# Performance work log

Hardware: AMD Instinct MI355X
Metric: run time of the kernel (lower is better)

The kernel has to match this reference:

```python
import jax, jax.numpy as jnp
import numpy as np


def setup_inputs() -> dict:
    key = jax.random.key(0)
    ks = jax.random.split(key, 6)
    b, t, k, h = 8, 128, 128, 4
    q_x = jax.random.normal(ks[0], (b, t, k), dtype=jnp.float32)
    kv_x = jax.random.normal(ks[1], (b, t, t - 1, k), dtype=jnp.float32)
    s = 1.0 / np.sqrt(k).astype(np.float32)
    Wk = jax.random.normal(ks[2], (k, k), dtype=jnp.float32) * s  # tokeys.weight
    Wq = jax.random.normal(ks[3], (k, k), dtype=jnp.float32) * s  # toqueries.weight
    Wv = jax.random.normal(ks[4], ((1 + k) * h, 2 * k), dtype=jnp.float32) * (1.0 / np.sqrt(2 * k).astype(np.float32))  # tovalues.weight
    bv = jax.random.normal(ks[5], ((1 + k) * h,), dtype=jnp.float32) * 0.01  # tovalues.bias
    return dict(q_x=q_x, kv_x=kv_x, Wk=Wk, Wq=Wq, Wv=Wv, bv=bv)


def reference(q_x, kv_x, Wk, Wq, Wv, bv):
    # kv_x: (b, t, t-1, k); q_x: (b, t, k)
    b, t, m, k = kv_x.shape  # m == t - 1
    h = Wv.shape[0] // (k + 1)
    # torch Linear: y = x @ W.T
    keys = jnp.einsum('btmk,jk->btmj', kv_x, Wk)          # (b,t,m,k)
    queries = jnp.einsum('btk,jk->btj', q_x, Wq)          # (b,t,k)
    queries = jnp.broadcast_to(queries[:, :, None, :], (b, t, m, k))
    value_input = jnp.concatenate([keys, queries], axis=-1)  # (b,t,m,2k)
    vals = jnp.einsum('btmc,oc->btmo', value_input, Wv) + bv  # (b,t,m,(1+k)h)
    vals = vals.reshape(b, t, m, h, k + 1)
    score = vals[..., 0]        # (b,t,m,h)
    values = vals[..., 1:]      # (b,t,m,h,k)
    w = jax.nn.softmax(score, axis=2)  # softmax over the t-1 (pair) axis
    x = jnp.einsum('btmh,btmhk->bthk', w, values)  # weighted sum over pairs
    return x.reshape(b, t, h * k)
```

## Files before the change

kernel.cpp:

```cpp
#include <hip/hip_runtime.h>

#define KD 128
#define NH 4
#define MM 127
#define NO 516

#define OFF_W1S 0
#define OFF_WC  512
#define OFF_C   (512 + 131072)

__global__ void precompute_w(const float* __restrict__ Wk,
                             const float* __restrict__ Wq,
                             const float* __restrict__ Wv,
                             float* __restrict__ ws) {
    int o = blockIdx.x;
    int k = threadIdx.x;
    const float* wvrow = Wv + o * 256;
    float acc1 = 0.f, acc2 = 0.f;
    #pragma unroll 8
    for (int j = 0; j < 128; ++j) {
        acc1 += wvrow[j]       * Wk[j * 128 + k];
        acc2 += wvrow[128 + j] * Wq[j * 128 + k];
    }
    int h = o / 129;
    int r = o - h * 129;
    if (r == 0) {
        ws[OFF_W1S + h * 128 + k] = acc1;
    } else {
        int dd = r - 1;
        float* dst = ws + OFF_WC + (size_t)(h * 128 + dd) * 256;
        dst[k]       = acc1;
        dst[128 + k] = acc2;
    }
}

__global__ __launch_bounds__(256, 4)
void attn_csum(const float* __restrict__ kv_x, float* __restrict__ ws) {
    __shared__ float ssc[512];
    __shared__ float swt[512];
    __shared__ float cpart[8][512];

    const int bt  = blockIdx.x;
    const int tid = threadIdx.x;
    const int dq  = tid & 31;
    const int g   = tid >> 5;

    float4 w1s[NH];
    #pragma unroll
    for (int h = 0; h < NH; ++h)
        w1s[h] = *(const float4*)(ws + OFF_W1S + h * KD + dq * 4);

    const float4* src = (const float4*)(kv_x + (size_t)bt * MM * KD);
    float4 kvr[16];
    #pragma unroll
    for (int k = 0; k < 16; ++k) {
        int idx = tid + k * 256;
        if (idx < MM * 32) kvr[k] = src[idx];
        else               kvr[k] = make_float4(0.f, 0.f, 0.f, 0.f);
    }

    const int bit4 = (tid >> 4) & 1;
    const int bit3 = (tid >> 3) & 1;
    const int myh  = bit4 * 2 + bit3;
    #pragma unroll
    for (int k = 0; k < 16; ++k) {
        float4 kv4 = kvr[k];
        float p0 = kv4.x*w1s[0].x + kv4.y*w1s[0].y + kv4.z*w1s[0].z + kv4.w*w1s[0].w;
        float p1 = kv4.x*w1s[1].x + kv4.y*w1s[1].y + kv4.z*w1s[1].z + kv4.w*w1s[1].w;
        float p2 = kv4.x*w1s[2].x + kv4.y*w1s[2].y + kv4.z*w1s[2].z + kv4.w*w1s[2].w;
        float p3 = kv4.x*w1s[3].x + kv4.y*w1s[3].y + kv4.z*w1s[3].z + kv4.w*w1s[3].w;
        float x = bit4 ? p0 : p2;
        float y = bit4 ? p1 : p3;
        float a = (bit4 ? p2 : p0) + __shfl_xor(x, 16);
        float b = (bit4 ? p3 : p1) + __shfl_xor(y, 16);
        float z = bit3 ? a : b;
        float v = (bit3 ? b : a) + __shfl_xor(z, 8);
        v += __shfl_xor(v, 4);
        v += __shfl_xor(v, 2);
        v += __shfl_xor(v, 1);
        int m = g + 8 * k;
        if ((tid & 7) == 0 && m < MM) ssc[m * 4 + myh] = v;
    }
    __syncthreads();

    {
        int h = tid >> 6, lane = tid & 63;
        float v0 = ssc[lane * 4 + h];
        bool has1 = (lane + 64) < MM;
        float v1 = has1 ? ssc[(lane + 64) * 4 + h] : -1e30f;
        float mx = fmaxf(v0, v1);
        #pragma unroll
        for (int off = 32; off; off >>= 1) mx = fmaxf(mx, __shfl_xor(mx, off));
        float e0 = __expf(v0 - mx);
        float e1 = has1 ? __expf(v1 - mx) : 0.f;
        float s = e0 + e1;
        #pragma unroll
        for (int off = 32; off; off >>= 1) s += __shfl_xor(s, off);
        float inv = 1.f / s;
        swt[lane * 4 + h] = e0 * inv;
        swt[(lane + 64) * 4 + h] = has1 ? e1 * inv : 0.f;
    }
    __syncthreads();

    float4 cacc[NH];
    #pragma unroll
    for (int h = 0; h < NH; ++h) cacc[h] = make_float4(0.f, 0.f, 0.f, 0.f);
    #pragma unroll
    for (int k = 0; k < 16; ++k) {
        int m = g + 8 * k;
        float4 wv  = *(const float4*)&swt[m * 4];
        float4 kv4 = kvr[k];
        cacc[0].x += wv.x*kv4.x; cacc[0].y += wv.x*kv4.y; cacc[0].z += wv.x*kv4.z; cacc[0].w += wv.x*kv4.w;
        cacc[1].x += wv.y*kv4.x; cacc[1].y += wv.y*kv4.y; cacc[1].z += wv.y*kv4.z; cacc[1].w += wv.y*kv4.w;
        cacc[2].x += wv.z*kv4.x; cacc[2].y += wv.z*kv4.y; cacc[2].z += wv.z*kv4.z; cacc[2].w += wv.z*kv4.w;
        cacc[3].x += wv.w*kv4.x; cacc[3].y += wv.w*kv4.y; cacc[3].z += wv.w*kv4.z; cacc[3].w += wv.w*kv4.w;
    }
    #pragma unroll
    for (int h = 0; h < NH; ++h)
        *(float4*)&cpart[g][h * KD + dq * 4] = cacc[h];
    __syncthreads();

    float* cdst = ws + OFF_C + (size_t)bt * 512;
    #pragma unroll
    for (int rep = 0; rep < 2; ++rep) {
        int o = tid + rep * 256;
        float s = 0.f;
        #pragma unroll
        for (int gg = 0; gg < 8; ++gg) s += cpart[gg][o];
        cdst[o] = s;
    }
}

#define BM 32
#define BN 64
#define BK 64

__global__ __launch_bounds__(256, 2)
void proj_out(const float* __restrict__ q_x,
              const float* __restrict__ bv,
              const float* __restrict__ ws,
              float* __restrict__ out) {
    __shared__ float sA[BM][BK + 4];
    __shared__ float sB[BK][BN + 4];

    const int r0  = blockIdx.x * BM;
    const int dd0 = blockIdx.y * BN;
    const int h   = blockIdx.z;
    const int tid = threadIdx.x;
    const int tx  = tid & 15;
    const int ty  = tid >> 4;
    const float* cmat = ws + OFF_C;
    const float* Wc   = ws + OFF_WC;

    float acc[2][4];
    #pragma unroll
    for (int i = 0; i < 2; ++i)
        #pragma unroll
        for (int j = 0; j < 4; ++j) acc[i][j] = 0.f;

    for (int ks = 0; ks < 4; ++ks) {
        int kk0 = ks * BK;
        const float* Abase; int Astride;
        if (kk0 < 128) { Abase = cmat + h * KD + kk0; Astride = 512; }
        else           { Abase = q_x + (kk0 - 128);   Astride = KD;  }
        #pragma unroll
        for (int i = 0; i < 2; ++i) {
            int idx = tid + i * 256;
            int r = idx >> 4, c4 = idx & 15;
            float4 v = *(const float4*)(Abase + (size_t)(r0 + r) * Astride + c4 * 4);
            *(float4*)&sA[r][c4 * 4] = v;
        }
        #pragma unroll
        for (int i = 0; i < 4; ++i) {
            int idx = tid + i * 256;
            int dd = idx >> 4, c4 = idx & 15;
            float4 v = *(const float4*)(Wc + (size_t)(h * KD + dd0 + dd) * 256 + kk0 + c4 * 4);
            sB[c4 * 4 + 0][dd] = v.x;
            sB[c4 * 4 + 1][dd] = v.y;
            sB[c4 * 4 + 2][dd] = v.z;
            sB[c4 * 4 + 3][dd] = v.w;
        }
        __syncthreads();
        #pragma unroll 8
        for (int c = 0; c < BK; ++c) {
            float a0 = sA[ty * 2 + 0][c];
            float a1 = sA[ty * 2 + 1][c];
            float4 b4 = *(const float4*)&sB[c][tx * 4];
            acc[0][0] += a0 * b4.x; acc[0][1] += a0 * b4.y; acc[0][2] += a0 * b4.z; acc[0][3] += a0 * b4.w;
            acc[1][0] += a1 * b4.x; acc[1][1] += a1 * b4.y; acc[1][2] += a1 * b4.z; acc[1][3] += a1 * b4.w;
        }
        __syncthreads();
    }
    float bb[4];
    #pragma unroll
    for (int j = 0; j < 4; ++j) bb[j] = bv[h * 129 + 1 + dd0 + tx * 4 + j];
    #pragma unroll
    for (int i = 0; i < 2; ++i) {
        float4 v;
        v.x = acc[i][0] + bb[0];
        v.y = acc[i][1] + bb[1];
        v.z = acc[i][2] + bb[2];
        v.w = acc[i][3] + bb[3];
        *(float4*)(out + (size_t)(r0 + ty * 2 + i) * 512 + h * KD + dd0 + tx * 4) = v;
    }
}

extern "C" void kernel_launch(void* const* d_in, const int* in_sizes, int n_in,
                              void* d_out, int out_size, void* d_ws, size_t ws_size,
                              hipStream_t stream) {
    const float* q_x  = (const float*)d_in[0];
    const float* kv_x = (const float*)d_in[1];
    const float* Wk   = (const float*)d_in[2];
    const float* Wq   = (const float*)d_in[3];
    const float* Wv   = (const float*)d_in[4];
    const float* bv   = (const float*)d_in[5];
    float* out = (float*)d_out;
    float* ws  = (float*)d_ws;

    int bt = in_sizes[0] / KD;

    hipLaunchKernelGGL(precompute_w, dim3(NO), dim3(128), 0, stream, Wk, Wq, Wv, ws);
    hipLaunchKernelGGL(attn_csum, dim3(bt), dim3(256), 0, stream, kv_x, ws);
    hipLaunchKernelGGL(proj_out, dim3(bt / BM, KD / BN, NH), dim3(256), 0, stream,
                       q_x, bv, ws, out);
}
```

Measured before the change: 42.42 us.

## Store combined value weights transposed and halve proj_out tile width

The precomputed combined weight matrix is now written in transposed (k-major) layout, so proj_out can load B tiles with direct float4 copies into shared memory instead of four scalar transposing stores. The output tile width drops from 64 to 32 columns, with each thread computing one row by four columns. This doubles the grid and raises the occupancy hint, aiming for more parallelism on this small GEMM. The cost is less register reuse per thread and strided scalar writes in precompute_w.

```diff
diff --git a/kernel.cpp b/kernel.cpp
--- a/kernel.cpp
+++ b/kernel.cpp
@@ -28,9 +28,8 @@
         ws[OFF_W1S + h * 128 + k] = acc1;
     } else {
         int dd = r - 1;
-        float* dst = ws + OFF_WC + (size_t)(h * 128 + dd) * 256;
-        dst[k]       = acc1;
-        dst[128 + k] = acc2;
+        ws[OFF_WC + (size_t)(h * 256 + k) * 128 + dd]       = acc1;
+        ws[OFF_WC + (size_t)(h * 256 + 128 + k) * 128 + dd] = acc2;
     }
 }
 
@@ -132,10 +131,10 @@
 }
 
 #define BM 32
-#define BN 64
+#define BN 32
 #define BK 64
 
-__global__ __launch_bounds__(256, 2)
+__global__ __launch_bounds__(256, 4)
 void proj_out(const float* __restrict__ q_x,
               const float* __restrict__ bv,
               const float* __restrict__ ws,
@@ -147,16 +146,12 @@
     const int dd0 = blockIdx.y * BN;
     const int h   = blockIdx.z;
     const int tid = threadIdx.x;
-    const int tx  = tid & 15;
-    const int ty  = tid >> 4;
+    const int tx  = tid & 7;
+    const int ty  = tid >> 3;
     const float* cmat = ws + OFF_C;
-    const float* Wc   = ws + OFF_WC;
-
-    float acc[2][4];
-    #pragma unroll
-    for (int i = 0; i < 2; ++i)
-        #pragma unroll
-        for (int j = 0; j < 4; ++j) acc[i][j] = 0.f;
+    const float* Wct  = ws + OFF_WC;
+
+    float acc[4] = {0.f, 0.f, 0.f, 0.f};
 
     for (int ks = 0; ks < 4; ++ks) {
         int kk0 = ks * BK;
@@ -167,42 +162,31 @@
         for (int i = 0; i < 2; ++i) {
             int idx = tid + i * 256;
             int r = idx >> 4, c4 = idx & 15;
-            float4 v = *(const float4*)(Abase + (size_t)(r0 + r) * Astride + c4 * 4);
-            *(float4*)&sA[r][c4 * 4] = v;
+            *(float4*)&sA[r][c4 * 4] =
+                *(const float4*)(Abase + (size_t)(r0 + r) * Astride + c4 * 4);
         }
         #pragma unroll
-        for (int i = 0; i < 4; ++i) {
+        for (int i = 0; i < 2; ++i) {
             int idx = tid + i * 256;
-            int dd = idx >> 4, c4 = idx & 15;
-            float4 v = *(const float4*)(Wc + (size_t)(h * KD + dd0 + dd) * 256 + kk0 + c4 * 4);
-            sB[c4 * 4 + 0][dd] = v.x;
-            sB[c4 * 4 + 1][dd] = v.y;
-            sB[c4 * 4 + 2][dd] = v.z;
-            sB[c4 * 4 + 3][dd] = v.w;
+            int c = idx >> 3, d4 = idx & 7;
+            *(float4*)&sB[c][d4 * 4] =
+                *(const float4*)(Wct + (size_t)(h * 256 + kk0 + c) * 128 + dd0 + d4 * 4);
         }
         __syncthreads();
         #pragma unroll 8
         for (int c = 0; c < BK; ++c) {
-            float a0 = sA[ty * 2 + 0][c];
-            float a1 = sA[ty * 2 + 1][c];
+            float a = sA[ty][c];
             float4 b4 = *(const float4*)&sB[c][tx * 4];
-            acc[0][0] += a0 * b4.x; acc[0][1] += a0 * b4.y; acc[0][2] += a0 * b4.z; acc[0][3] += a0 * b4.w;
-            acc[1][0] += a1 * b4.x; acc[1][1] += a1 * b4.y; acc[1][2] += a1 * b4.z; acc[1][3] += a1 * b4.w;
+            acc[0] += a * b4.x; acc[1] += a * b4.y; acc[2] += a * b4.z; acc[3] += a * b4.w;
         }
         __syncthreads();
     }
-    float bb[4];
-    #pragma unroll
-    for (int j = 0; j < 4; ++j) bb[j] = bv[h * 129 + 1 + dd0 + tx * 4 + j];
-    #pragma unroll
-    for (int i = 0; i < 2; ++i) {
-        float4 v;
-        v.x = acc[i][0] + bb[0];
-        v.y = acc[i][1] + bb[1];
-        v.z = acc[i][2] + bb[2];
-        v.w = acc[i][3] + bb[3];
-        *(float4*)(out + (size_t)(r0 + ty * 2 + i) * 512 + h * KD + dd0 + tx * 4) = v;
-    }
+    float4 v;
+    v.x = acc[0] + bv[h * 129 + 1 + dd0 + tx * 4 + 0];
+    v.y = acc[1] + bv[h * 129 + 1 + dd0 + tx * 4 + 1];
+    v.z = acc[2] + bv[h * 129 + 1 + dd0 + tx * 4 + 2];
+    v.w = acc[3] + bv[h * 129 + 1 + dd0 + tx * 4 + 3];
+    *(float4*)(out + (size_t)(r0 + ty) * 512 + h * KD + dd0 + tx * 4) = v;
 }
 
 extern "C" void kernel_launch(void* const* d_in, const int* in_sizes, int n_in,
```

New measurement: 39.25 us. -7.5%, faster.

## Fuse weight precompute into attention kernel and transpose combined weight layout

Applied to the files above, without the earlier changes.

Merges the weight-precompute kernel into the attention kernel as extra leading blocks, removing one launch and the dependency between them. Each attention block now recomputes the four score-weight vectors (Wv·Wk rows) in shared memory instead of reading them from workspace, which adds redundant per-block work. The combined weight matrix is stored transposed so proj_out loads it with direct float4 stores, while the A tile is now transposed into shared memory and read as float2.

```diff
diff --git a/kernel.cpp b/kernel.cpp
--- a/kernel.cpp
+++ b/kernel.cpp
@@ -3,61 +3,74 @@
 #define KD 128
 #define NH 4
 #define MM 127
-#define NO 516
-
-#define OFF_W1S 0
-#define OFF_WC  512
-#define OFF_C   (512 + 131072)
-
-__global__ void precompute_w(const float* __restrict__ Wk,
-                             const float* __restrict__ Wq,
-                             const float* __restrict__ Wv,
-                             float* __restrict__ ws) {
-    int o = blockIdx.x;
-    int k = threadIdx.x;
-    const float* wvrow = Wv + o * 256;
-    float acc1 = 0.f, acc2 = 0.f;
-    #pragma unroll 8
-    for (int j = 0; j < 128; ++j) {
-        acc1 += wvrow[j]       * Wk[j * 128 + k];
-        acc2 += wvrow[128 + j] * Wq[j * 128 + k];
-    }
-    int h = o / 129;
-    int r = o - h * 129;
-    if (r == 0) {
-        ws[OFF_W1S + h * 128 + k] = acc1;
-    } else {
+#define NPRE 516
+
+#define OFF_WC 0
+#define OFF_C  131072
+
+__global__ __launch_bounds__(256, 4)
+void attn_fused(const float* __restrict__ kv_x,
+                const float* __restrict__ Wk,
+                const float* __restrict__ Wq,
+                const float* __restrict__ Wv,
+                float* __restrict__ ws) {
+    const int bid = blockIdx.x;
+    const int tid = threadIdx.x;
+
+    if (bid < NPRE) {
+        int o = bid;
+        int h = o / 129, r = o - h * 129;
+        if (r == 0) return;
         int dd = r - 1;
-        float* dst = ws + OFF_WC + (size_t)(h * 128 + dd) * 256;
-        dst[k]       = acc1;
-        dst[128 + k] = acc2;
-    }
-}
-
-__global__ __launch_bounds__(256, 4)
-void attn_csum(const float* __restrict__ kv_x, float* __restrict__ ws) {
+        int which = tid >> 7, k = tid & 127;
+        const float* W = which ? Wq : Wk;
+        const float* wvrow = Wv + (size_t)o * 256 + which * 128;
+        float acc = 0.f;
+        #pragma unroll 8
+        for (int j = 0; j < 128; ++j)
+            acc += wvrow[j] * W[j * 128 + k];
+        ws[OFF_WC + (size_t)(h * 256 + which * 128 + k) * 128 + dd] = acc;
+        return;
+    }
+
+    __shared__ float sW1s[NH * KD];
     __shared__ float ssc[512];
     __shared__ float swt[512];
     __shared__ float cpart[8][512];
 
-    const int bt  = blockIdx.x;
-    const int tid = threadIdx.x;
-    const int dq  = tid & 31;
-    const int g   = tid >> 5;
-
-    float4 w1s[NH];
-    #pragma unroll
-    for (int h = 0; h < NH; ++h)
-        w1s[h] = *(const float4*)(ws + OFF_W1S + h * KD + dq * 4);
+    const int bt = bid - NPRE;
+    const int dq = tid & 31;
+    const int g  = tid >> 5;
 
     const float4* src = (const float4*)(kv_x + (size_t)bt * MM * KD);
     float4 kvr[16];
     #pragma unroll
     for (int k = 0; k < 16; ++k) {
         int idx = tid + k * 256;
-        if (idx < MM * 32) kvr[k] = src[idx];
-        else               kvr[k] = make_float4(0.f, 0.f, 0.f, 0.f);
-    }
+        kvr[k] = (idx < MM * 32) ? src[idx] : make_float4(0.f, 0.f, 0.f, 0.f);
+    }
+
+    {
+        int h0 = tid >> 7;
+        int k  = tid & 127;
+        const float* wv0 = Wv + (size_t)(129 * h0) * 256;
+        const float* wv2 = Wv + (size_t)(129 * (h0 + 2)) * 256;
+        float a0 = 0.f, a1 = 0.f;
+        #pragma unroll 8
+        for (int j = 0; j < 128; ++j) {
+            float wk = Wk[j * 128 + k];
+            a0 += wv0[j] * wk;
+            a1 += wv2[j] * wk;
+        }
+        sW1s[h0 * 128 + k]       = a0;
+        sW1s[(h0 + 2) * 128 + k] = a1;
+    }
+    __syncthreads();
+
+    float4 w1s[NH];
+    #pragma unroll
+    for (int h = 0; h < NH; ++h)
+        w1s[h] = *(const float4*)&sW1s[h * KD + dq * 4];
 
     const int bit4 = (tid >> 4) & 1;
     const int bit3 = (tid >> 3) & 1;
@@ -134,14 +147,16 @@
 #define BM 32
 #define BN 64
 #define BK 64
+#define AP 34
+#define BP 68
 
 __global__ __launch_bounds__(256, 2)
 void proj_out(const float* __restrict__ q_x,
               const float* __restrict__ bv,
               const float* __restrict__ ws,
               float* __restrict__ out) {
-    __shared__ float sA[BM][BK + 4];
-    __shared__ float sB[BK][BN + 4];
+    __shared__ float sAT[BK][AP];
+    __shared__ float sB[BK][BP];
 
     const int r0  = blockIdx.x * BM;
     const int dd0 = blockIdx.y * BN;
@@ -150,7 +165,7 @@
     const int tx  = tid & 15;
     const int ty  = tid >> 4;
     const float* cmat = ws + OFF_C;
-    const float* Wc   = ws + OFF_WC;
+    const float* Wct  = ws + OFF_WC;
 
     float acc[2][4];
     #pragma unroll
@@ -168,26 +183,27 @@
             int idx = tid + i * 256;
             int r = idx >> 4, c4 = idx & 15;
             float4 v = *(const float4*)(Abase + (size_t)(r0 + r) * Astride + c4 * 4);
-            *(float4*)&sA[r][c4 * 4] = v;
+            sAT[c4 * 4 + 0][r] = v.x;
+            sAT[c4 * 4 + 1][r] = v.y;
+            sAT[c4 * 4 + 2][r] = v.z;
+            sAT[c4 * 4 + 3][r] = v.w;
         }
         #pragma unroll
         for (int i = 0; i < 4; ++i) {
             int idx = tid + i * 256;
-            int dd = idx >> 4, c4 = idx & 15;
-            float4 v = *(const float4*)(Wc + (size_t)(h * KD + dd0 + dd) * 256 + kk0 + c4 * 4);
-            sB[c4 * 4 + 0][dd] = v.x;
-            sB[c4 * 4 + 1][dd] = v.y;
-            sB[c4 * 4 + 2][dd] = v.z;
-            sB[c4 * 4 + 3][dd] = v.w;
+            int c = idx >> 4, d4 = idx & 15;
+            *(float4*)&sB[c][d4 * 4] =
+                *(const float4*)(Wct + (size_t)(h * 256 + kk0 + c) * 128 + dd0 + d4 * 4);
         }
         __syncthreads();
         #pragma unroll 8
         for (int c = 0; c < BK; ++c) {
-            float a0 = sA[ty * 2 + 0][c];
-            float a1 = sA[ty * 2 + 1][c];
+            float2 a  = *(const float2*)&sAT[c][ty * 2];
             float4 b4 = *(const float4*)&sB[c][tx * 4];
-            acc[0][0] += a0 * b4.x; acc[0][1] += a0 * b4.y; acc[0][2] += a0 * b4.z; acc[0][3] += a0 * b4.w;
-            acc[1][0] += a1 * b4.x; acc[1][1] += a1 * b4.y; acc[1][2] += a1 * b4.z; acc[1][3] += a1 * b4.w;
+            acc[0][0] += a.x * b4.x; acc[0][1] += a.x * b4.y;
+            acc[0][2] += a.x * b4.z; acc[0][3] += a.x * b4.w;
+            acc[1][0] += a.y * b4.x; acc[1][1] += a.y * b4.y;
+            acc[1][2] += a.y * b4.z; acc[1][3] += a.y * b4.w;
         }
         __syncthreads();
     }
@@ -219,8 +235,8 @@
 
     int bt = in_sizes[0] / KD;
 
-    hipLaunchKernelGGL(precompute_w, dim3(NO), dim3(128), 0, stream, Wk, Wq, Wv, ws);
-    hipLaunchKernelGGL(attn_csum, dim3(bt), dim3(256), 0, stream, kv_x, ws);
+    hipLaunchKernelGGL(attn_fused, dim3(NPRE + bt), dim3(256), 0, stream,
+                       kv_x, Wk, Wq, Wv, ws);
     hipLaunchKernelGGL(proj_out, dim3(bt / BM, KD / BN, NH), dim3(256), 0, stream,
                        q_x, bv, ws, out);
 }
```

After: 45.56 us. 1.07x slower.

## Stage kv tile in LDS and transpose Wc layout for GEMM loads

Applied to the files above, without the earlier changes.

attn_csum no longer keeps the 16 float4 kv values per thread live across the softmax. It stores the kv tile (about 65 KB) in shared memory and does the weighted sum with a per-head, split-m loop, which shrinks the partial-sum buffer. The precompute kernel now writes Wc transposed, so proj_out can load B tiles with float4 stores instead of scalar transposed stores. A is transposed into shared memory so the inner loop reads it as float2. The large LDS footprint lowers attn_csum's occupancy bound from 4 to 2 in exchange for lower register pressure, and the reduction loop becomes serial over m.

```diff
diff --git a/kernel.cpp b/kernel.cpp
--- a/kernel.cpp
+++ b/kernel.cpp
@@ -28,17 +28,17 @@
         ws[OFF_W1S + h * 128 + k] = acc1;
     } else {
         int dd = r - 1;
-        float* dst = ws + OFF_WC + (size_t)(h * 128 + dd) * 256;
-        dst[k]       = acc1;
-        dst[128 + k] = acc2;
-    }
-}
-
-__global__ __launch_bounds__(256, 4)
+        ws[OFF_WC + (size_t)(h * 256 + k) * 128 + dd]       = acc1;
+        ws[OFF_WC + (size_t)(h * 256 + 128 + k) * 128 + dd] = acc2;
+    }
+}
+
+__global__ __launch_bounds__(256, 2)
 void attn_csum(const float* __restrict__ kv_x, float* __restrict__ ws) {
+    __shared__ float skv[MM * KD];
     __shared__ float ssc[512];
     __shared__ float swt[512];
-    __shared__ float cpart[8][512];
+    __shared__ float cpart[2][512];
 
     const int bt  = blockIdx.x;
     const int tid = threadIdx.x;
@@ -51,35 +51,31 @@
         w1s[h] = *(const float4*)(ws + OFF_W1S + h * KD + dq * 4);
 
     const float4* src = (const float4*)(kv_x + (size_t)bt * MM * KD);
-    float4 kvr[16];
-    #pragma unroll
-    for (int k = 0; k < 16; ++k) {
-        int idx = tid + k * 256;
-        if (idx < MM * 32) kvr[k] = src[idx];
-        else               kvr[k] = make_float4(0.f, 0.f, 0.f, 0.f);
-    }
-
     const int bit4 = (tid >> 4) & 1;
     const int bit3 = (tid >> 3) & 1;
     const int myh  = bit4 * 2 + bit3;
+
     #pragma unroll
     for (int k = 0; k < 16; ++k) {
-        float4 kv4 = kvr[k];
-        float p0 = kv4.x*w1s[0].x + kv4.y*w1s[0].y + kv4.z*w1s[0].z + kv4.w*w1s[0].w;
-        float p1 = kv4.x*w1s[1].x + kv4.y*w1s[1].y + kv4.z*w1s[1].z + kv4.w*w1s[1].w;
-        float p2 = kv4.x*w1s[2].x + kv4.y*w1s[2].y + kv4.z*w1s[2].z + kv4.w*w1s[2].w;
-        float p3 = kv4.x*w1s[3].x + kv4.y*w1s[3].y + kv4.z*w1s[3].z + kv4.w*w1s[3].w;
+        int idx = tid + k * 256;
+        int m   = g + 8 * k;
+        bool valid = (m < MM);
+        float4 v = valid ? src[idx] : make_float4(0.f, 0.f, 0.f, 0.f);
+        if (valid) *(float4*)&skv[m * KD + dq * 4] = v;
+        float p0 = v.x*w1s[0].x + v.y*w1s[0].y + v.z*w1s[0].z + v.w*w1s[0].w;
+        float p1 = v.x*w1s[1].x + v.y*w1s[1].y + v.z*w1s[1].z + v.w*w1s[1].w;
+        float p2 = v.x*w1s[2].x + v.y*w1s[2].y + v.z*w1s[2].z + v.w*w1s[2].w;
+        float p3 = v.x*w1s[3].x + v.y*w1s[3].y + v.z*w1s[3].z + v.w*w1s[3].w;
         float x = bit4 ? p0 : p2;
         float y = bit4 ? p1 : p3;
         float a = (bit4 ? p2 : p0) + __shfl_xor(x, 16);
         float b = (bit4 ? p3 : p1) + __shfl_xor(y, 16);
         float z = bit3 ? a : b;
-        float v = (bit3 ? b : a) + __shfl_xor(z, 8);
-        v += __shfl_xor(v, 4);
-        v += __shfl_xor(v, 2);
-        v += __shfl_xor(v, 1);
-        int m = g + 8 * k;
-        if ((tid & 7) == 0 && m < MM) ssc[m * 4 + myh] = v;
+        float vr = (bit3 ? b : a) + __shfl_xor(z, 8);
+        vr += __shfl_xor(vr, 4);
+        vr += __shfl_xor(vr, 2);
+        vr += __shfl_xor(vr, 1);
+        if ((tid & 7) == 0 && valid) ssc[m * 4 + myh] = vr;
     }
     __syncthreads();
 
@@ -98,50 +94,49 @@
         for (int off = 32; off; off >>= 1) s += __shfl_xor(s, off);
         float inv = 1.f / s;
         swt[lane * 4 + h] = e0 * inv;
-        swt[(lane + 64) * 4 + h] = has1 ? e1 * inv : 0.f;
+        if (has1) swt[(lane + 64) * 4 + h] = e1 * inv;
     }
     __syncthreads();
 
-    float4 cacc[NH];
-    #pragma unroll
-    for (int h = 0; h < NH; ++h) cacc[h] = make_float4(0.f, 0.f, 0.f, 0.f);
-    #pragma unroll
-    for (int k = 0; k < 16; ++k) {
-        int m = g + 8 * k;
-        float4 wv  = *(const float4*)&swt[m * 4];
-        float4 kv4 = kvr[k];
-        cacc[0].x += wv.x*kv4.x; cacc[0].y += wv.x*kv4.y; cacc[0].z += wv.x*kv4.z; cacc[0].w += wv.x*kv4.w;
-        cacc[1].x += wv.y*kv4.x; cacc[1].y += wv.y*kv4.y; cacc[1].z += wv.y*kv4.z; cacc[1].w += wv.y*kv4.w;
-        cacc[2].x += wv.z*kv4.x; cacc[2].y += wv.z*kv4.y; cacc[2].z += wv.z*kv4.z; cacc[2].w += wv.z*kv4.w;
-        cacc[3].x += wv.w*kv4.x; cacc[3].y += wv.w*kv4.y; cacc[3].z += wv.w*kv4.z; cacc[3].w += wv.w*kv4.w;
-    }
-    #pragma unroll
-    for (int h = 0; h < NH; ++h)
-        *(float4*)&cpart[g][h * KD + dq * 4] = cacc[h];
+    {
+        const int ch = (tid >> 5) & 3;
+        const int mh = tid >> 7;
+        const int m0 = mh ? 64 : 0;
+        const int m1 = mh ? MM : 64;
+        float4 fa = make_float4(0.f, 0.f, 0.f, 0.f);
+        #pragma unroll 8
+        for (int m = m0; m < m1; ++m) {
+            float w = swt[m * 4 + ch];
+            float4 kq = *(const float4*)&skv[m * KD + dq * 4];
+            fa.x += w * kq.x; fa.y += w * kq.y;
+            fa.z += w * kq.z; fa.w += w * kq.w;
+        }
+        *(float4*)&cpart[mh][ch * KD + dq * 4] = fa;
+    }
     __syncthreads();
 
-    float* cdst = ws + OFF_C + (size_t)bt * 512;
-    #pragma unroll
-    for (int rep = 0; rep < 2; ++rep) {
-        int o = tid + rep * 256;
-        float s = 0.f;
-        #pragma unroll
-        for (int gg = 0; gg < 8; ++gg) s += cpart[gg][o];
-        cdst[o] = s;
+    if (tid < 128) {
+        float4 a = *(const float4*)&cpart[0][tid * 4];
+        float4 b = *(const float4*)&cpart[1][tid * 4];
+        float4 s;
+        s.x = a.x + b.x; s.y = a.y + b.y; s.z = a.z + b.z; s.w = a.w + b.w;
+        *(float4*)(ws + OFF_C + (size_t)bt * 512 + tid * 4) = s;
     }
 }
 
 #define BM 32
 #define BN 64
 #define BK 64
+#define AP 34
+#define BP 68
 
 __global__ __launch_bounds__(256, 2)
 void proj_out(const float* __restrict__ q_x,
               const float* __restrict__ bv,
               const float* __restrict__ ws,
               float* __restrict__ out) {
-    __shared__ float sA[BM][BK + 4];
-    __shared__ float sB[BK][BN + 4];
+    __shared__ float sAT[BK][AP];
+    __shared__ float sB[BK][BP];
 
     const int r0  = blockIdx.x * BM;
     const int dd0 = blockIdx.y * BN;
@@ -150,7 +145,7 @@
     const int tx  = tid & 15;
     const int ty  = tid >> 4;
     const float* cmat = ws + OFF_C;
-    const float* Wc   = ws + OFF_WC;
+    const float* Wct  = ws + OFF_WC;
 
     float acc[2][4];
     #pragma unroll
@@ -168,26 +163,27 @@
             int idx = tid + i * 256;
             int r = idx >> 4, c4 = idx & 15;
             float4 v = *(const float4*)(Abase + (size_t)(r0 + r) * Astride + c4 * 4);
-            *(float4*)&sA[r][c4 * 4] = v;
+            sAT[c4 * 4 + 0][r] = v.x;
+            sAT[c4 * 4 + 1][r] = v.y;
+            sAT[c4 * 4 + 2][r] = v.z;
+            sAT[c4 * 4 + 3][r] = v.w;
         }
         #pragma unroll
         for (int i = 0; i < 4; ++i) {
             int idx = tid + i * 256;
-            int dd = idx >> 4, c4 = idx & 15;
-            float4 v = *(const float4*)(Wc + (size_t)(h * KD + dd0 + dd) * 256 + kk0 + c4 * 4);
-            sB[c4 * 4 + 0][dd] = v.x;
-            sB[c4 * 4 + 1][dd] = v.y;
-            sB[c4 * 4 + 2][dd] = v.z;
-            sB[c4 * 4 + 3][dd] = v.w;
+            int c = idx >> 4, d4 = idx & 15;
+            *(float4*)&sB[c][d4 * 4] =
+                *(const float4*)(Wct + (size_t)(h * 256 + kk0 + c) * 128 + dd0 + d4 * 4);
         }
         __syncthreads();
         #pragma unroll 8
         for (int c = 0; c < BK; ++c) {
-            float a0 = sA[ty * 2 + 0][c];
-            float a1 = sA[ty * 2 + 1][c];
+            float2 a  = *(const float2*)&sAT[c][ty * 2];
             float4 b4 = *(const float4*)&sB[c][tx * 4];
-            acc[0][0] += a0 * b4.x; acc[0][1] += a0 * b4.y; acc[0][2] += a0 * b4.z; acc[0][3] += a0 * b4.w;
-            acc[1][0] += a1 * b4.x; acc[1][1] += a1 * b4.y; acc[1][2] += a1 * b4.z; acc[1][3] += a1 * b4.w;
+            acc[0][0] += a.x * b4.x; acc[0][1] += a.x * b4.y;
+            acc[0][2] += a.x * b4.z; acc[0][3] += a.x * b4.w;
+            acc[1][0] += a.y * b4.x; acc[1][1] += a.y * b4.y;
+            acc[1][2] += a.y * b4.z; acc[1][3] += a.y * b4.w;
         }
         __syncthreads();
     }
```

Measured after the change: 47.93 us. 13.0% more time.
